# Kernel optimization log

Hardware: AMD Instinct MI355X
Metric: run time of the kernel (lower is better)

Reference implementation:

```python
import jax, jax.numpy as jnp
import numpy as np

B, V, DIN, DOUT, S = 32768, 43, 64, 64, 2  # batch, local_graph_vert=43, dims, n_supports


def setup_inputs() -> dict:
    key = jax.random.key(0)
    k1, k2, k3 = jax.random.split(key, 3)
    x = jax.random.normal(k1, (B, V, DIN), dtype=jnp.float32)
    adj = jax.random.uniform(k2, (S, V, V), dtype=jnp.float32)
    # glorot init per support weight matrix
    scale = jnp.sqrt(6.0 / (DIN + DOUT)).astype(jnp.float32)
    W = jax.random.uniform(k3, (S, DIN, DOUT), minval=-1.0, maxval=1.0, dtype=jnp.float32) * scale
    b = jnp.zeros((DOUT,), dtype=jnp.float32)
    return {"x": x, "adj": adj, "W": W, "b": b}


def reference(x, adj, W, b):
    # For each support s: pre_s = x @ W_s  (einsum 'bvi,sio->sbvo')
    #                     out += adj_s @ pre_s  (einsum 'suv,sbvo->buo')
    # Fused multi-support reduction in one einsum; dropout rate is 0 (dropout=False).
    out = jnp.einsum('suv,bvi,sio->buo', adj, x, W)  # [B, V, DOUT]
    out = out + b
    return jax.nn.relu(out)
```

## Files before the change

kernel.cpp:

```cpp
#include <hip/hip_runtime.h>
#include <stdint.h>


#define BATCH 32768
#define NV 43
#define DIN 64
#define DOUT 64
#define NS 2
#define XEL (NV * DIN)
#define NCHUNK (XEL / 4)

#define SX 72
#define SP 104

typedef __attribute__((ext_vector_type(8))) short short8;
typedef __attribute__((ext_vector_type(4))) float f32x4;
typedef __attribute__((ext_vector_type(4))) unsigned short ushort4_t;

__device__ __forceinline__ unsigned short f2bf(float f) {
    union { float f; unsigned int u; } x;
    x.f = f;
    unsigned int r = x.u + 0x7FFFu + ((x.u >> 16) & 1u);
    return (unsigned short)(r >> 16);
}

__device__ __forceinline__ ushort4_t cvt4(f32x4 v) {
    ushort4_t r;
    r[0] = f2bf(v[0]); r[1] = f2bf(v[1]);
    r[2] = f2bf(v[2]); r[3] = f2bf(v[3]);
    return r;
}

__global__ void __launch_bounds__(256, 4) lgconv_kernel(
    const float* __restrict__ xg,
    const float* __restrict__ adjg,
    const float* __restrict__ wg,
    const float* __restrict__ bg,
    float* __restrict__ outg)
{
    __shared__ __align__(16) unsigned short s_x[2][48 * SX];
    __shared__ __align__(16) unsigned short s_pre[DOUT * SP];
    __shared__ __align__(16) unsigned short s_a[48 * SP];

    const int tid  = threadIdx.x;
    const int wv   = tid >> 6;
    const int lane = tid & 63;
    const int quad = lane >> 4;
    const int l16  = lane & 15;

    {
        unsigned short* p = &s_x[0][0];
        for (int t = tid; t < 2 * 48 * SX; t += 256) p[t] = 0;
        for (int t = tid; t < DOUT * SP; t += 256) s_pre[t] = 0;
        for (int t = tid; t < 48 * SP; t += 256) s_a[t] = 0;
    }
    __syncthreads();

    for (int t = tid; t < NS * NV * NV; t += 256) {
        int s  = t / (NV * NV);
        int rc = t - s * NV * NV;
        int r  = rc / NV;
        int c  = rc - r * NV;
        s_a[r * SP + s * 48 + c] = f2bf(adjg[t]);
    }

    short8 wfrag[NS][2];
    for (int s = 0; s < NS; ++s)
        for (int kc = 0; kc < 2; ++kc) {
            short8 f;
            #pragma unroll
            for (int j = 0; j < 8; ++j) {
                int i = kc * 32 + quad * 8 + j;
                f[j] = (short)f2bf(wg[(s * DIN + i) * DOUT + wv * 16 + l16]);
            }
            wfrag[s][kc] = f;
        }
    const float biasv = bg[wv * 16 + l16];

    {
        const float* src = xg + (size_t)blockIdx.x * XEL;
        #pragma unroll
        for (int c = 0; c < 3; ++c) {
            int flat = c * 256 + tid;
            if (flat < NCHUNK) {
                f32x4 u = *(const f32x4*)(src + (size_t)flat * 4);
                *(ushort4_t*)(&s_x[0][(flat >> 4) * SX + (flat & 15) * 4]) = cvt4(u);
            }
        }
    }
    __syncthreads();

    const int orow = wv * 16 + l16;
    int cur = 0;
    for (int b = blockIdx.x; b < BATCH; b += gridDim.x) {
        const int  bn = b + gridDim.x;
        const bool hn = (bn < BATCH);

        f32x4 pf0, pf1, pf2;
        const float* srcn = xg + (size_t)bn * XEL;
        if (hn) {
            pf0 = *(const f32x4*)(srcn + (size_t)(tid) * 4);
            pf1 = *(const f32x4*)(srcn + (size_t)(256 + tid) * 4);
            if (tid < NCHUNK - 512)
                pf2 = *(const f32x4*)(srcn + (size_t)(512 + tid) * 4);
        }

        const unsigned short* xl = &s_x[cur][0];
        short8 afrag[3][2];
        #pragma unroll
        for (int mt = 0; mt < 3; ++mt)
            #pragma unroll
            for (int kc = 0; kc < 2; ++kc)
                afrag[mt][kc] = *(const short8*)(xl + (mt * 16 + l16) * SX + kc * 32 + quad * 8);

        #pragma unroll
        for (int s = 0; s < NS; ++s) {
            #pragma unroll
            for (int mt = 0; mt < 3; ++mt) {
                f32x4 c = {0.f, 0.f, 0.f, 0.f};
                c = __builtin_amdgcn_mfma_f32_16x16x32_bf16(afrag[mt][0], wfrag[s][0], c, 0, 0, 0);
                c = __builtin_amdgcn_mfma_f32_16x16x32_bf16(afrag[mt][1], wfrag[s][1], c, 0, 0, 0);
                *(ushort4_t*)(&s_pre[orow * SP + s * 48 + mt * 16 + quad * 4]) = cvt4(c);
            }
        }
        __builtin_amdgcn_s_waitcnt(0xc07f);
        __builtin_amdgcn_sched_barrier(0);

        f32x4 oacc[3];
        #pragma unroll
        for (int mt = 0; mt < 3; ++mt) oacc[mt] = (f32x4){0.f, 0.f, 0.f, 0.f};
        #pragma unroll
        for (int kc = 0; kc < 3; ++kc) {
            short8 bfr = *(const short8*)(&s_pre[orow * SP + kc * 32 + quad * 8]);
            #pragma unroll
            for (int mt = 0; mt < 3; ++mt) {
                short8 afr = *(const short8*)(&s_a[(mt * 16 + l16) * SP + kc * 32 + quad * 8]);
                oacc[mt] = __builtin_amdgcn_mfma_f32_16x16x32_bf16(afr, bfr, oacc[mt], 0, 0, 0);
            }
        }

        if (hn) {
            unsigned short* xn = &s_x[cur ^ 1][0];
            *(ushort4_t*)(&xn[(tid >> 4) * SX + (tid & 15) * 4]) = cvt4(pf0);
            {
                int flat = 256 + tid;
                *(ushort4_t*)(&xn[(flat >> 4) * SX + (flat & 15) * 4]) = cvt4(pf1);
            }
            if (tid < NCHUNK - 512) {
                int flat = 512 + tid;
                *(ushort4_t*)(&xn[(flat >> 4) * SX + (flat & 15) * 4]) = cvt4(pf2);
            }
        }

        float* op = outg + (size_t)b * (NV * DOUT) + orow;
        #pragma unroll
        for (int mt = 0; mt < 3; ++mt) {
            #pragma unroll
            for (int r = 0; r < 4; ++r) {
                int u = mt * 16 + quad * 4 + r;
                if (u < NV)
                    op[u * DOUT] = fmaxf(oacc[mt][r] + biasv, 0.f);
            }
        }
        __syncthreads();
        cur ^= 1;
    }
}

extern "C" void kernel_launch(void* const* d_in, const int* in_sizes, int n_in,
                              void* d_out, int out_size, void* d_ws, size_t ws_size,
                              hipStream_t stream) {
    (void)in_sizes; (void)n_in; (void)d_ws; (void)ws_size; (void)out_size;
    const float* xg   = (const float*)d_in[0];
    const float* adjg = (const float*)d_in[1];
    const float* wg   = (const float*)d_in[2];
    const float* bg   = (const float*)d_in[3];
    float* outg = (float*)d_out;

    dim3 grid(1024), block(256);
    hipLaunchKernelGGL(lgconv_kernel, grid, block, 0, stream, xg, adjg, wg, bg, outg);
}
```

Baseline: 591.4 us.

## Load x fragments directly from global into registers, drop LDS staging

Each wave now prefetches its MFMA A-fragments for the next batch item straight from global memory into registers and packs them to bf16 with hardware packed conversions. This replaces the shared-memory double buffer for x, removing the LDS writes and reads for x and the per-iteration block barrier. The cost is that every wave redundantly loads the full x tile, which quadruples L2/L1 traffic for x, and it uses more registers (48 VGPRs of prefetch) at occupancy 4.

```diff
diff --git a/kernel.cpp b/kernel.cpp
--- a/kernel.cpp
+++ b/kernel.cpp
@@ -1,4 +1,5 @@
 #include <hip/hip_runtime.h>
+#include <hip/hip_bf16.h>
 #include <stdint.h>
 
 
@@ -7,10 +8,8 @@
 #define DIN 64
 #define DOUT 64
 #define NS 2
-#define XEL (NV * DIN)
-#define NCHUNK (XEL / 4)
+#define NWAVES 4
 
-#define SX 72
 #define SP 104
 
 typedef __attribute__((ext_vector_type(8))) short short8;
@@ -24,11 +23,24 @@
     return (unsigned short)(r >> 16);
 }
 
+__device__ __forceinline__ unsigned int pk2(float lo, float hi) {
+    __hip_bfloat162 h = __float22bfloat162_rn(make_float2(lo, hi));
+    union { __hip_bfloat162 h; unsigned int u; } c;
+    c.h = h;
+    return c.u;
+}
+
+__device__ __forceinline__ short8 pack8(f32x4 a, f32x4 b) {
+    union { short8 s; unsigned int u[4]; } r;
+    r.u[0] = pk2(a[0], a[1]); r.u[1] = pk2(a[2], a[3]);
+    r.u[2] = pk2(b[0], b[1]); r.u[3] = pk2(b[2], b[3]);
+    return r.s;
+}
+
 __device__ __forceinline__ ushort4_t cvt4(f32x4 v) {
-    ushort4_t r;
-    r[0] = f2bf(v[0]); r[1] = f2bf(v[1]);
-    r[2] = f2bf(v[2]); r[3] = f2bf(v[3]);
-    return r;
+    union { ushort4_t v; unsigned int u[2]; } r;
+    r.u[0] = pk2(v[0], v[1]); r.u[1] = pk2(v[2], v[3]);
+    return r.v;
 }
 
 __global__ void __launch_bounds__(256, 4) lgconv_kernel(
@@ -38,7 +50,6 @@
     const float* __restrict__ bg,
     float* __restrict__ outg)
 {
-    __shared__ __align__(16) unsigned short s_x[2][48 * SX];
     __shared__ __align__(16) unsigned short s_pre[DOUT * SP];
     __shared__ __align__(16) unsigned short s_a[48 * SP];
 
@@ -48,12 +59,8 @@
     const int quad = lane >> 4;
     const int l16  = lane & 15;
 
-    {
-        unsigned short* p = &s_x[0][0];
-        for (int t = tid; t < 2 * 48 * SX; t += 256) p[t] = 0;
-        for (int t = tid; t < DOUT * SP; t += 256) s_pre[t] = 0;
-        for (int t = tid; t < 48 * SP; t += 256) s_a[t] = 0;
-    }
+    for (int t = tid; t < DOUT * SP; t += 256) s_pre[t] = 0;
+    for (int t = tid; t < 48 * SP; t += 256) s_a[t] = 0;
     __syncthreads();
 
     for (int t = tid; t < NS * NV * NV; t += 256) {
@@ -76,42 +83,56 @@
             wfrag[s][kc] = f;
         }
     const float biasv = bg[wv * 16 + l16];
-
-    {
-        const float* src = xg + (size_t)blockIdx.x * XEL;
-        #pragma unroll
-        for (int c = 0; c < 3; ++c) {
-            int flat = c * 256 + tid;
-            if (flat < NCHUNK) {
-                f32x4 u = *(const f32x4*)(src + (size_t)flat * 4);
-                *(ushort4_t*)(&s_x[0][(flat >> 4) * SX + (flat & 15) * 4]) = cvt4(u);
-            }
-        }
-    }
     __syncthreads();
 
     const int orow = wv * 16 + l16;
-    int cur = 0;
+
+    const float* prow[3];
+    bool mval[3];
+    #pragma unroll
+    for (int mt = 0; mt < 3; ++mt) {
+        int m = mt * 16 + l16;
+        mval[mt] = (m < NV);
+        prow[mt] = xg + ((size_t)blockIdx.x * NV + m) * DIN + quad * 8;
+    }
+
+    f32x4 pf[3][2][2];
+    #pragma unroll
+    for (int mt = 0; mt < 3; ++mt)
+        #pragma unroll
+        for (int kc = 0; kc < 2; ++kc)
+            #pragma unroll
+            for (int h = 0; h < 2; ++h) {
+                pf[mt][kc][h] = (f32x4){0.f, 0.f, 0.f, 0.f};
+                if (mval[mt])
+                    pf[mt][kc][h] = *(const f32x4*)(prow[mt] + kc * 32 + h * 4);
+            }
+
+    float* op = outg + (size_t)blockIdx.x * (NV * DOUT) + orow;
+    const size_t xadv = (size_t)gridDim.x * NV * DIN;
+    const size_t oadv = (size_t)gridDim.x * NV * DOUT;
+
     for (int b = blockIdx.x; b < BATCH; b += gridDim.x) {
-        const int  bn = b + gridDim.x;
-        const bool hn = (bn < BATCH);
-
-        f32x4 pf0, pf1, pf2;
-        const float* srcn = xg + (size_t)bn * XEL;
-        if (hn) {
-            pf0 = *(const f32x4*)(srcn + (size_t)(tid) * 4);
-            pf1 = *(const f32x4*)(srcn + (size_t)(256 + tid) * 4);
-            if (tid < NCHUNK - 512)
-                pf2 = *(const f32x4*)(srcn + (size_t)(512 + tid) * 4);
-        }
-
-        const unsigned short* xl = &s_x[cur][0];
         short8 afrag[3][2];
         #pragma unroll
         for (int mt = 0; mt < 3; ++mt)
             #pragma unroll
             for (int kc = 0; kc < 2; ++kc)
-                afrag[mt][kc] = *(const short8*)(xl + (mt * 16 + l16) * SX + kc * 32 + quad * 8);
+                afrag[mt][kc] = pack8(pf[mt][kc][0], pf[mt][kc][1]);
+
+        const bool hn = (b + (int)gridDim.x) < BATCH;
+        #pragma unroll
+        for (int mt = 0; mt < 3; ++mt) prow[mt] += xadv;
+        #pragma unroll
+        for (int mt = 0; mt < 3; ++mt)
+            #pragma unroll
+            for (int kc = 0; kc < 2; ++kc)
+                #pragma unroll
+                for (int h = 0; h < 2; ++h) {
+                    pf[mt][kc][h] = (f32x4){0.f, 0.f, 0.f, 0.f};
+                    if (hn && mval[mt])
+                        pf[mt][kc][h] = *(const f32x4*)(prow[mt] + kc * 32 + h * 4);
+                }
 
         #pragma unroll
         for (int s = 0; s < NS; ++s) {
@@ -139,31 +160,16 @@
             }
         }
 
-        if (hn) {
-            unsigned short* xn = &s_x[cur ^ 1][0];
-            *(ushort4_t*)(&xn[(tid >> 4) * SX + (tid & 15) * 4]) = cvt4(pf0);
-            {
-                int flat = 256 + tid;
-                *(ushort4_t*)(&xn[(flat >> 4) * SX + (flat & 15) * 4]) = cvt4(pf1);
-            }
-            if (tid < NCHUNK - 512) {
-                int flat = 512 + tid;
-                *(ushort4_t*)(&xn[(flat >> 4) * SX + (flat & 15) * 4]) = cvt4(pf2);
-            }
-        }
-
-        float* op = outg + (size_t)b * (NV * DOUT) + orow;
         #pragma unroll
         for (int mt = 0; mt < 3; ++mt) {
             #pragma unroll
             for (int r = 0; r < 4; ++r) {
                 int u = mt * 16 + quad * 4 + r;
                 if (u < NV)
-                    op[u * DOUT] = fmaxf(oacc[mt][r] + biasv, 0.f);
+                    op[(size_t)u * DOUT] = fmaxf(oacc[mt][r] + biasv, 0.f);
             }
         }
-        __syncthreads();
-        cur ^= 1;
+        op += oadv;
     }
 }
 
```

Measured after the change: 676.0 us. +14.3%, slower.
